# Kernel tuning notes

Measured on AMD Instinct MI355X. Metric: run time of the kernel, lower is better.

## Reference

```python
import jax, jax.numpy as jnp
import numpy as np

B, H, G, N, D = 1, 32, 64, 128, 128   # batch, heads, blocks, block_len, head_dim
S = 256                               # sketch dim (multiple of 16)
BIT_PACK = 8


def setup_inputs() -> dict:
    key = jax.random.key(0)
    k1, k2, k3 = jax.random.split(key, 3)
    data = jax.random.normal(k1, (B, H, G, N, D), dtype=jnp.float32)
    # binary per-channel outlier mask, float {0,1}, shape matches data.shape[:3] + (D,)
    outlier_mask = jax.random.randint(k2, (B, H, G, D), 0, 2).astype(jnp.float32)
    # proj_dir_quant = proj_dir_score.T -> shape (S, D)
    proj_dir_quant = jax.random.normal(k3, (S, D), dtype=jnp.float32)
    return {"data": data, "outlier_mask": outlier_mask, "proj_dir_quant": proj_dir_quant}


def _pack_bits(sketch):
    # sketch: (..., S). Reshape to (..., S//8, 8), threshold at 0, pack sign bits into uint8.
    x = sketch.reshape(*sketch.shape[:-1], -1, BIT_PACK)
    enc = (2 ** jnp.arange(BIT_PACK, dtype=jnp.int32))  # [1,2,4,...,128]
    packed = ((x > 0).astype(jnp.int32) * enc).sum(axis=-1)  # max 255, fits uint8
    return packed.astype(jnp.uint8)


def reference(data, outlier_mask, proj_dir_quant):
    s = proj_dir_quant.shape[0]
    m = outlier_mask[..., None, :]                     # (B,H,G,1,D) broadcast over tokens
    key_outlier = data * m
    key_inlier = data * (1.0 - m)
    # '...nd,sd->...ns' : sign-random-projection sketch
    sk_outlier = jnp.einsum('bhgnd,sd->bhgns', key_outlier, proj_dir_quant)
    sk_inlier = jnp.einsum('bhgnd,sd->bhgns', key_inlier, proj_dir_quant)
    hash_inlier = _pack_bits(sk_inlier)                # (B,H,G,N,S//8)
    hash_outlier = _pack_bits(sk_outlier)[..., : s // 16]  # (B,H,G,N,S//16)
    return (hash_inlier, hash_outlier)
```

## Files before the change

kernel.cpp:

```cpp
#include <hip/hip_runtime.h>

#define NB_HG 2048
#define DIM_N 128
#define DIM_D 128
#define DIM_S 256
#define PH 32


__global__ void transpose_proj_kernel(const float* __restrict__ proj,
                                      float* __restrict__ projT)
{
    const int d = blockIdx.x;
    const int s = threadIdx.x;
    projT[d * DIM_S + s] = proj[s * DIM_D + d];
}

template<bool TP>
__global__ __launch_bounds__(256)
void qjl_sketch_kernel(const float* __restrict__ data,
                       const float* __restrict__ mask,
                       const float* __restrict__ pmat,
                       int* __restrict__ out)
{
    __shared__ float Xt[PH * DIM_N];
    __shared__ int   cidx[DIM_D];
    __shared__ int   wcnt[2];

    const int type = blockIdx.x;
    const int hg   = blockIdx.y;
    const int tid  = threadIdx.x;

    bool sel = false; int pos = 0, w = 0;
    if (tid < 128) {
        const float m = mask[hg * DIM_D + tid];
        sel = (type == 2) ? (m != 0.0f) : (m == 0.0f);
        const unsigned long long bal = __ballot(sel);
        const int lane = tid & 63;
        w = tid >> 6;
        if (lane == 0) wcnt[w] = __popcll(bal);
        pos = __popcll(bal & ((1ull << lane) - 1ull));
    }
    __syncthreads();
    if (sel) cidx[pos + (w ? wcnt[0] : 0)] = tid;
    __syncthreads();
    const int K = wcnt[0] + wcnt[1];

    const int tn = tid & 15;
    const int ts = tid >> 4;
    const int C0 = 4 * tn;
    const int s0 = ((type == 1) ? 128 : 0) + ts * 8;

    float acc[8][8];
    #pragma unroll
    for (int j = 0; j < 8; ++j)
        #pragma unroll
        for (int i = 0; i < 8; ++i) acc[j][i] = 0.0f;

    const int cl_s = tid & 31;
    const int nh   = tid >> 5;
    const int pcs  = 4 * (cl_s & 7);
    float* srow = &Xt[cl_s * DIM_N];

    auto STAGE = [&](int base, int kp) {
        if (cl_s < kp) {
            const int dg = cidx[base + cl_s];
            const float* Xs = data + (size_t)hg * (DIM_N * DIM_D) + dg;
            #pragma unroll
            for (int g = 0; g < 4; ++g) {
                const int n0 = nh * 16 + g * 4;
                float4 v;
                v.x = Xs[(size_t)(n0 + 0) * DIM_D];
                v.y = Xs[(size_t)(n0 + 1) * DIM_D];
                v.z = Xs[(size_t)(n0 + 2) * DIM_D];
                v.w = Xs[(size_t)(n0 + 3) * DIM_D];
                *reinterpret_cast<float4*>(&srow[n0 ^ pcs]) = v;
            }
        }
    };

    auto COMPUTE = [&](int base, int kp) {
        #pragma unroll 2
        for (int cl = 0; cl < kp; ++cl) {
            const int dg = cidx[base + cl];
            float bv[8];
            if (TP) {
                const float* pr = pmat + (size_t)dg * DIM_S + s0;
                const float4 b0 = *reinterpret_cast<const float4*>(pr);
                const float4 b1 = *reinterpret_cast<const float4*>(pr + 4);
                bv[0]=b0.x; bv[1]=b0.y; bv[2]=b0.z; bv[3]=b0.w;
                bv[4]=b1.x; bv[5]=b1.y; bv[6]=b1.z; bv[7]=b1.w;
            } else {
                #pragma unroll
                for (int j = 0; j < 8; ++j)
                    bv[j] = pmat[(size_t)(s0 + j) * DIM_D + dg];
            }

            const int P = C0 ^ (4 * (cl & 7));
            const float* r = &Xt[cl * DIM_N + P];
            const float4 q0 = *reinterpret_cast<const float4*>(r);
            const float4 q1 = *reinterpret_cast<const float4*>(r + 64);

            #pragma unroll
            for (int j = 0; j < 8; ++j) {
                acc[j][0] = fmaf(bv[j], q0.x, acc[j][0]);
                acc[j][1] = fmaf(bv[j], q0.y, acc[j][1]);
                acc[j][2] = fmaf(bv[j], q0.z, acc[j][2]);
                acc[j][3] = fmaf(bv[j], q0.w, acc[j][3]);
                acc[j][4] = fmaf(bv[j], q1.x, acc[j][4]);
                acc[j][5] = fmaf(bv[j], q1.y, acc[j][5]);
                acc[j][6] = fmaf(bv[j], q1.z, acc[j][6]);
                acc[j][7] = fmaf(bv[j], q1.w, acc[j][7]);
            }
        }
    };

    for (int base = 0; base < K; base += PH) {
        const int kp = (K - base < PH) ? (K - base) : PH;
        if (base) __syncthreads();
        STAGE(base, kp);
        __syncthreads();
        COMPUTE(base, kp);
    }

    const size_t inl_total = (size_t)NB_HG * DIM_N * 32;
    #pragma unroll
    for (int i = 0; i < 8; ++i) {
        int byte = 0;
        #pragma unroll
        for (int j = 0; j < 8; ++j)
            if (acc[j][i] > 0.0f) byte |= (1 << j);
        const int n = (i < 4) ? (C0 + i) : (64 + C0 + (i - 4));
        size_t idx;
        if (type == 2)
            idx = inl_total + ((size_t)hg * DIM_N + n) * 16 + ts;
        else
            idx = ((size_t)hg * DIM_N + n) * 32 + (type == 1 ? 16 : 0) + ts;
        out[idx] = byte;
    }
}

extern "C" void kernel_launch(void* const* d_in, const int* in_sizes, int n_in,
                              void* d_out, int out_size, void* d_ws, size_t ws_size,
                              hipStream_t stream) {
    const float* data = (const float*)d_in[0];
    const float* mask = (const float*)d_in[1];
    const float* proj = (const float*)d_in[2];
    int* out = (int*)d_out;

    dim3 grid(3, NB_HG);
    const size_t tp_bytes = (size_t)DIM_D * DIM_S * sizeof(float);
    if (ws_size >= tp_bytes) {
        float* projT = (float*)d_ws;
        transpose_proj_kernel<<<DIM_D, DIM_S, 0, stream>>>(proj, projT);
        qjl_sketch_kernel<true><<<grid, 256, 0, stream>>>(data, mask, projT, out);
    } else {
        qjl_sketch_kernel<false><<<grid, 256, 0, stream>>>(data, mask, proj, out);
    }
}
```

Baseline: 208.9 us.

## Merge three per-type blocks into one block staging full data tile once

Each (head,block) pair is now handled by a single workgroup that loads the entire 128x128 data tile into shared memory once. It then runs three passes over it: inlier low half, inlier high half, and outlier. Before, three separate workgroups each reloaded the selected columns. This removes redundant global reads, but uses 64KB of LDS per block, which lowers occupancy, and the grid shrinks to 2048 blocks of serial work.

```diff
diff --git a/kernel.cpp b/kernel.cpp
--- a/kernel.cpp
+++ b/kernel.cpp
@@ -4,7 +4,6 @@
 #define DIM_N 128
 #define DIM_D 128
 #define DIM_S 256
-#define PH 32
 
 
 __global__ void transpose_proj_kernel(const float* __restrict__ proj,
@@ -22,83 +21,87 @@
                        const float* __restrict__ pmat,
                        int* __restrict__ out)
 {
-    __shared__ float Xt[PH * DIM_N];
-    __shared__ int   cidx[DIM_D];
-    __shared__ int   wcnt[2];
+    __shared__ float Xt[DIM_D * DIM_N];
+    __shared__ int   din[DIM_D];
+    __shared__ int   dout[DIM_D];
+    __shared__ int   win[2];
 
-    const int type = blockIdx.x;
-    const int hg   = blockIdx.y;
-    const int tid  = threadIdx.x;
+    const int hg  = blockIdx.x;
+    const int tid = threadIdx.x;
 
-    bool sel = false; int pos = 0, w = 0;
+    const int  lane = tid & 63;
+    const int  w    = tid >> 6;
+    bool is_in = false; int rank_in = 0;
     if (tid < 128) {
         const float m = mask[hg * DIM_D + tid];
-        sel = (type == 2) ? (m != 0.0f) : (m == 0.0f);
-        const unsigned long long bal = __ballot(sel);
-        const int lane = tid & 63;
-        w = tid >> 6;
-        if (lane == 0) wcnt[w] = __popcll(bal);
-        pos = __popcll(bal & ((1ull << lane) - 1ull));
+        is_in = (m == 0.0f);
+        const unsigned long long bal = __ballot(is_in);
+        if (lane == 0) win[w] = __popcll(bal);
+        rank_in = __popcll(bal & ((1ull << lane) - 1ull));
     }
     __syncthreads();
-    if (sel) cidx[pos + (w ? wcnt[0] : 0)] = tid;
+    const int Kin = win[0] + win[1];
+    if (tid < 128) {
+        if (is_in) din [rank_in          + (w ? win[0]        : 0)] = tid;
+        else       dout[(lane - rank_in) + (w ? (64 - win[0]) : 0)] = tid;
+    }
+
+    {
+        const int d  = tid & 127;
+        const int nh = tid >> 7;
+        const float* Xs = data + (size_t)hg * (DIM_N * DIM_D) + d;
+        const int pcs = 4 * (d & 7);
+        float* row = &Xt[d * DIM_N];
+        #pragma unroll
+        for (int g = 0; g < 16; ++g) {
+            const int n0 = g * 8 + nh * 4;
+            float4 v;
+            v.x = Xs[(size_t)(n0 + 0) * DIM_D];
+            v.y = Xs[(size_t)(n0 + 1) * DIM_D];
+            v.z = Xs[(size_t)(n0 + 2) * DIM_D];
+            v.w = Xs[(size_t)(n0 + 3) * DIM_D];
+            *reinterpret_cast<float4*>(&row[n0 ^ pcs]) = v;
+        }
+    }
     __syncthreads();
-    const int K = wcnt[0] + wcnt[1];
 
     const int tn = tid & 15;
     const int ts = tid >> 4;
     const int C0 = 4 * tn;
-    const int s0 = ((type == 1) ? 128 : 0) + ts * 8;
+    const int sl = ts * 8;
+    const size_t inl_total = (size_t)NB_HG * DIM_N * 32;
 
-    float acc[8][8];
-    #pragma unroll
-    for (int j = 0; j < 8; ++j)
+    auto PASS = [&](const int* __restrict__ list, int cnt, int sbase, int typ) {
+        float acc[8][8];
         #pragma unroll
-        for (int i = 0; i < 8; ++i) acc[j][i] = 0.0f;
+        for (int j = 0; j < 8; ++j)
+            #pragma unroll
+            for (int i = 0; i < 8; ++i) acc[j][i] = 0.0f;
 
-    const int cl_s = tid & 31;
-    const int nh   = tid >> 5;
-    const int pcs  = 4 * (cl_s & 7);
-    float* srow = &Xt[cl_s * DIM_N];
-
-    auto STAGE = [&](int base, int kp) {
-        if (cl_s < kp) {
-            const int dg = cidx[base + cl_s];
-            const float* Xs = data + (size_t)hg * (DIM_N * DIM_D) + dg;
-            #pragma unroll
-            for (int g = 0; g < 4; ++g) {
-                const int n0 = nh * 16 + g * 4;
-                float4 v;
-                v.x = Xs[(size_t)(n0 + 0) * DIM_D];
-                v.y = Xs[(size_t)(n0 + 1) * DIM_D];
-                v.z = Xs[(size_t)(n0 + 2) * DIM_D];
-                v.w = Xs[(size_t)(n0 + 3) * DIM_D];
-                *reinterpret_cast<float4*>(&srow[n0 ^ pcs]) = v;
+        #pragma unroll 4
+        for (int ci = 0; ci < cnt; ++ci) {
+            const int dl = list[ci];
+            float4 b0, b1;
+            if (TP) {
+                const float* pr = pmat + (size_t)dl * DIM_S + sbase + sl;
+                b0 = *reinterpret_cast<const float4*>(pr);
+                b1 = *reinterpret_cast<const float4*>(pr + 4);
+            } else {
+                b0.x = pmat[(size_t)(sbase + sl + 0) * DIM_D + dl];
+                b0.y = pmat[(size_t)(sbase + sl + 1) * DIM_D + dl];
+                b0.z = pmat[(size_t)(sbase + sl + 2) * DIM_D + dl];
+                b0.w = pmat[(size_t)(sbase + sl + 3) * DIM_D + dl];
+                b1.x = pmat[(size_t)(sbase + sl + 4) * DIM_D + dl];
+                b1.y = pmat[(size_t)(sbase + sl + 5) * DIM_D + dl];
+                b1.z = pmat[(size_t)(sbase + sl + 6) * DIM_D + dl];
+                b1.w = pmat[(size_t)(sbase + sl + 7) * DIM_D + dl];
             }
-        }
-    };
-
-    auto COMPUTE = [&](int base, int kp) {
-        #pragma unroll 2
-        for (int cl = 0; cl < kp; ++cl) {
-            const int dg = cidx[base + cl];
-            float bv[8];
-            if (TP) {
-                const float* pr = pmat + (size_t)dg * DIM_S + s0;
-                const float4 b0 = *reinterpret_cast<const float4*>(pr);
-                const float4 b1 = *reinterpret_cast<const float4*>(pr + 4);
-                bv[0]=b0.x; bv[1]=b0.y; bv[2]=b0.z; bv[3]=b0.w;
-                bv[4]=b1.x; bv[5]=b1.y; bv[6]=b1.z; bv[7]=b1.w;
-            } else {
-                #pragma unroll
-                for (int j = 0; j < 8; ++j)
-                    bv[j] = pmat[(size_t)(s0 + j) * DIM_D + dg];
-            }
-
-            const int P = C0 ^ (4 * (cl & 7));
-            const float* r = &Xt[cl * DIM_N + P];
+            const int pcs = 4 * (dl & 7);
+            const int P   = C0 ^ pcs;
+            const float* r = &Xt[dl * DIM_N + P];
             const float4 q0 = *reinterpret_cast<const float4*>(r);
             const float4 q1 = *reinterpret_cast<const float4*>(r + 64);
+            const float bv[8] = {b0.x, b0.y, b0.z, b0.w, b1.x, b1.y, b1.z, b1.w};
 
             #pragma unroll
             for (int j = 0; j < 8; ++j) {
@@ -112,31 +115,27 @@
                 acc[j][7] = fmaf(bv[j], q1.w, acc[j][7]);
             }
         }
+
+        #pragma unroll
+        for (int i = 0; i < 8; ++i) {
+            int byte = 0;
+            #pragma unroll
+            for (int j = 0; j < 8; ++j)
+                if (acc[j][i] > 0.0f) byte |= (1 << j);
+            const int n = (i < 4) ? (C0 + i) : (64 + C0 + (i - 4));
+            size_t idx;
+            if (typ == 2)
+                idx = inl_total + ((size_t)hg * DIM_N + n) * 16 + ts;
+            else
+                idx = ((size_t)hg * DIM_N + n) * 32 + (typ == 1 ? 16 : 0) + ts;
+            out[idx] = byte;
+        }
     };
 
-    for (int base = 0; base < K; base += PH) {
-        const int kp = (K - base < PH) ? (K - base) : PH;
-        if (base) __syncthreads();
-        STAGE(base, kp);
-        __syncthreads();
-        COMPUTE(base, kp);
-    }
+    PASS(din,  Kin,         0,   0);
+    PASS(din,  Kin,         128, 1);
+    PASS(dout, DIM_D - Kin, 0,   2);
 
-    const size_t inl_total = (size_t)NB_HG * DIM_N * 32;
-    #pragma unroll
-    for (int i = 0; i < 8; ++i) {
-        int byte = 0;
-        #pragma unroll
-        for (int j = 0; j < 8; ++j)
-            if (acc[j][i] > 0.0f) byte |= (1 << j);
-        const int n = (i < 4) ? (C0 + i) : (64 + C0 + (i - 4));
-        size_t idx;
-        if (type == 2)
-            idx = inl_total + ((size_t)hg * DIM_N + n) * 16 + ts;
-        else
-            idx = ((size_t)hg * DIM_N + n) * 32 + (type == 1 ? 16 : 0) + ts;
-        out[idx] = byte;
-    }
 }
 
 extern "C" void kernel_launch(void* const* d_in, const int* in_sizes, int n_in,
@@ -147,13 +146,12 @@
     const float* proj = (const float*)d_in[2];
     int* out = (int*)d_out;
 
-    dim3 grid(3, NB_HG);
     const size_t tp_bytes = (size_t)DIM_D * DIM_S * sizeof(float);
     if (ws_size >= tp_bytes) {
         float* projT = (float*)d_ws;
         transpose_proj_kernel<<<DIM_D, DIM_S, 0, stream>>>(proj, projT);
-        qjl_sketch_kernel<true><<<grid, 256, 0, stream>>>(data, mask, projT, out);
+        qjl_sketch_kernel<true><<<NB_HG, 256, 0, stream>>>(data, mask, projT, out);
     } else {
-        qjl_sketch_kernel<false><<<grid, 256, 0, stream>>>(data, mask, proj, out);
+        qjl_sketch_kernel<false><<<NB_HG, 256, 0, stream>>>(data, mask, proj, out);
     }
 }
```

Result: faster. 191.3 us (-8.4%).
